# Kernel tuning notes

Hardware: AMD Instinct MI355X
Metric: run time of the kernel (lower is better)

## Reference

```python
import jax, jax.numpy as jnp
import numpy as np

B, L, D, N, KEEP, HID = 64, 256, 128, 8192, 64, 1024
IN_DIM = D + KEEP * D + 1  # q + packed subset keys + log_count


def setup_inputs() -> dict:
    key = jax.random.key(0)
    ks = jax.random.split(key, 7)
    q = jax.random.normal(ks[0], (N, D), jnp.float32)
    k = jax.random.normal(ks[1], (B, L, D), jnp.float32)
    batch_idx = jax.random.randint(ks[2], (N,), 0, B)
    mask = jax.random.randint(ks[3], (N, L), 0, 2).astype(bool)
    count = jax.random.randint(ks[4], (N,), 0, L)
    W1 = jax.random.normal(ks[5], (IN_DIM, HID), jnp.float32) / np.sqrt(IN_DIM).astype(np.float32)
    b1 = jnp.zeros((HID,), jnp.float32)
    W2 = jax.random.normal(ks[6], (HID, 1), jnp.float32) / np.sqrt(HID).astype(np.float32)
    b2 = jnp.zeros((1,), jnp.float32)
    return dict(q=q, k=k, batch_idx=batch_idx, mask=mask, count=count,
                W1=W1, b1=b1, W2=W2, b2=b2)


def _pack_subset_keys(k, batch_idx, mask):
    # chain_k: [N, L, D] gather of per-chain key blocks
    chain_k = k[batch_idx]
    pos = jnp.arange(L, dtype=jnp.float32)
    # score = L - pos for masked positions, 0 otherwise -> topk picks first KEEP masked positions
    scores = mask.astype(jnp.float32) * (jnp.float32(L) - pos)[None, :]
    top_scores, top_idx = jax.lax.top_k(scores, KEEP)
    picked = top_scores > 0
    sortable = jnp.where(picked, top_idx, L)  # sentinel L for unpicked
    sortable = jnp.sort(sortable, axis=1)     # restore ascending position order
    picked = sortable < L
    safe_idx = jnp.where(picked, sortable, 0)
    packed = jnp.take_along_axis(chain_k, safe_idx[:, :, None], axis=1)  # [N, KEEP, D]
    packed = packed * picked[:, :, None].astype(packed.dtype)
    return packed.reshape(N, KEEP * D)


def reference(q, k, batch_idx, mask, count, W1, b1, W2, b2):
    packed = _pack_subset_keys(k, batch_idx, mask)
    log_count = jnp.log1p(count.astype(q.dtype))[:, None]
    feat = jnp.concatenate([q, packed, log_count], axis=-1)  # [N, IN_DIM]
    h = jax.nn.gelu(feat @ W1 + b1, approximate=False)       # torch GELU = exact erf
    return (h @ W2 + b2).squeeze(-1)                          # [N]
```

## Files before the change

kernel.cpp:

```cpp
#include <hip/hip_runtime.h>
#include <math.h>

#define N_ROWS 8192
#define B_CH   64
#define L_SEQ  256
#define D_DIM  128
#define KEEP   64
#define HID    1024
#define KTOT   8320

#define KOFF   (N_ROWS * D_DIM)
#define ZOFF   (KOFF + B_CH * L_SEQ * D_DIM)
#define BUF_ELEMS (ZOFF + 128)

typedef unsigned short ushort_t;
typedef __attribute__((ext_vector_type(8))) short  short8;
typedef __attribute__((ext_vector_type(4))) float  float4v;


__device__ __forceinline__ ushort_t f2bf(float f) {
    union { float f; unsigned int u; } v; v.f = f;
    unsigned int u = v.u;
    unsigned int r = u + 0x7fffu + ((u >> 16) & 1u);
    return (ushort_t)(r >> 16);
}

__device__ __forceinline__ void glds16(const void* g, void* l) {
    __builtin_amdgcn_global_load_lds(
        (const __attribute__((address_space(1))) unsigned int*)g,
        (__attribute__((address_space(3))) unsigned int*)l,
        16, 0, 0);
}

__global__ void init_out(float* __restrict__ out, const float* __restrict__ b2) {
    int i = blockIdx.x * blockDim.x + threadIdx.x;
    if (i < N_ROWS) out[i] = b2[0];
}

__global__ void conv_qk(const float* __restrict__ q, const float* __restrict__ k,
                        ushort_t* __restrict__ buf) {
    int c = blockIdx.x * blockDim.x + threadIdx.x;
    if (c >= BUF_ELEMS / 8) return;
    int e = c * 8;
    float4 x0, x1;
    if (e < KOFF) {
        const float4* s = (const float4*)(q + e);
        x0 = s[0]; x1 = s[1];
    } else if (e < ZOFF) {
        const float4* s = (const float4*)(k + (e - KOFF));
        x0 = s[0]; x1 = s[1];
    } else {
        x0 = make_float4(0.f, 0.f, 0.f, 0.f);
        x1 = x0;
    }
    union { ushort_t s[8]; uint4 v; } o;
    o.s[0] = f2bf(x0.x); o.s[1] = f2bf(x0.y); o.s[2] = f2bf(x0.z); o.s[3] = f2bf(x0.w);
    o.s[4] = f2bf(x1.x); o.s[5] = f2bf(x1.y); o.s[6] = f2bf(x1.z); o.s[7] = f2bf(x1.w);
    *(uint4*)(buf + e) = o.v;
}

__global__ void conv_w1t(const float* __restrict__ W1, ushort_t* __restrict__ w1t) {
    __shared__ float tile[64][65];
    const int k0 = blockIdx.x * 64, h0 = blockIdx.y * 64;
    const int t = threadIdx.x;
    const int hl = t & 63, kl = t >> 6;
#pragma unroll
    for (int i = 0; i < 16; ++i) {
        int kk = kl + i * 4;
        tile[kk][hl] = W1[(size_t)(k0 + kk) * HID + h0 + hl];
    }
    __syncthreads();
#pragma unroll
    for (int i = 0; i < 2; ++i) {
        int chunk = i * 256 + t;
        int h = chunk >> 3, piece = chunk & 7;
        union { ushort_t s[8]; uint4 v; } o;
#pragma unroll
        for (int j = 0; j < 8; ++j) o.s[j] = f2bf(tile[piece * 8 + j][h]);
        *(uint4*)(w1t + (size_t)(h0 + h) * KTOT + k0 + piece * 8) = o.v;
    }
}

__global__ void pack_idx(const int* __restrict__ mask, const int* __restrict__ batch_idx,
                         const int* __restrict__ count, int* __restrict__ srcLUT,
                         float* __restrict__ logc) {
    const int n = blockIdx.x, t = threadIdx.x;
    __shared__ int sidx[KEEP];
    __shared__ int wcnt[4];
    if (t < KEEP) sidx[t] = -1;
    __syncthreads();
    const int m = (mask[n * L_SEQ + t] != 0) ? 1 : 0;
    unsigned long long bal = __ballot(m);
    const int w = t >> 6, l = t & 63;
    if (l == 0) wcnt[w] = (int)__popcll(bal);
    __syncthreads();
    int base = 0;
    for (int i = 0; i < w; ++i) base += wcnt[i];
    const int rank = base + (int)__popcll(bal & ((1ull << l) - 1ull));
    if (m && rank < KEEP) sidx[rank] = t;
    __syncthreads();
    if (t < KEEP) {
        int s = sidx[t];
        int b = batch_idx[n];
        srcLUT[(t + 1) * N_ROWS + n] = (s >= 0) ? (KOFF + (b * L_SEQ + s) * D_DIM) : ZOFF;
    }
    if (t == 64) logc[n] = log1pf((float)count[n]);
    if (t == 65) srcLUT[n] = n * D_DIM;
}

__global__ __launch_bounds__(256, 2)
void gemm_mlp(const ushort_t* __restrict__ buf, const ushort_t* __restrict__ w1t,
              const int* __restrict__ srcLUT, const float* __restrict__ logc,
              const float* __restrict__ W1, const float* __restrict__ b1,
              const float* __restrict__ W2, float* __restrict__ out) {
    __shared__ ushort_t As[128 * 128];
    __shared__ ushort_t Bs[128 * 128];

    const int t = threadIdx.x;
    const int blkM = blockIdx.x, blkH = blockIdx.y;
    const int wave = t >> 6, lane = t & 63;
    const int wm = wave >> 1, wh = wave & 1;
    const int ln = lane & 15, quad = lane >> 4;

    float4v acc[4][4];
#pragma unroll
    for (int i = 0; i < 4; ++i)
#pragma unroll
        for (int j = 0; j < 4; ++j)
#pragma unroll
            for (int r = 0; r < 4; ++r) acc[i][j][r] = 0.0f;

    const int tr = t >> 4;
    const int slot = t & 15;
    const int pg = slot ^ tr;
    ushort_t* lA = As + t * 8;
    ushort_t* lB = Bs + t * 8;
    const ushort_t* gB[8];
#pragma unroll
    for (int i = 0; i < 8; ++i)
        gB[i] = w1t + (size_t)(blkH * 128 + i * 16 + tr) * KTOT + pg * 8;
    const int* lutBase = srcLUT + blkM * 128 + tr;

    int offA[8];
#pragma unroll
    for (int i = 0; i < 8; ++i) offA[i] = lutBase[i * 16];

    for (int bi = 0; bi < 65; ++bi) {
#pragma unroll
        for (int i = 0; i < 8; ++i) {
            glds16(buf + offA[i] + pg * 8, lA + i * 2048);
            glds16(gB[i] + bi * 128, lB + i * 2048);
        }
        int offN[8];
        if (bi < 64) {
#pragma unroll
            for (int i = 0; i < 8; ++i) offN[i] = lutBase[(bi + 1) * N_ROWS + i * 16];
        }
        __syncthreads();
#pragma unroll
        for (int kk = 0; kk < 4; ++kk) {
            short8 af[4], bfr[4];
#pragma unroll
            for (int mi = 0; mi < 4; ++mi) {
                const int row = wm * 64 + mi * 16 + ln;
                const int sl = (kk * 4 + quad) ^ ln;
                af[mi] = *(const short8*)(As + row * 128 + sl * 8);
            }
#pragma unroll
            for (int ni = 0; ni < 4; ++ni) {
                const int row = wh * 64 + ni * 16 + ln;
                const int sl = (kk * 4 + quad) ^ ln;
                bfr[ni] = *(const short8*)(Bs + row * 128 + sl * 8);
            }
#pragma unroll
            for (int mi = 0; mi < 4; ++mi)
#pragma unroll
                for (int ni = 0; ni < 4; ++ni)
                    acc[mi][ni] = __builtin_amdgcn_mfma_f32_16x16x32_bf16(
                        af[mi], bfr[ni], acc[mi][ni], 0, 0, 0);
        }
        __syncthreads();
#pragma unroll
        for (int i = 0; i < 8; ++i) offA[i] = offN[i];
    }

    const float* w1last = W1 + (size_t)KTOT * HID;
    float w1l[4], b1v[4], w2v[4];
#pragma unroll
    for (int ni = 0; ni < 4; ++ni) {
        int h = blkH * 128 + wh * 64 + ni * 16 + ln;
        w1l[ni] = w1last[h];
        b1v[ni] = b1[h];
        w2v[ni] = W2[h];
    }
    const int nbase = blkM * 128 + wm * 64 + quad * 4;
#pragma unroll
    for (int mi = 0; mi < 4; ++mi) {
#pragma unroll
        for (int rg = 0; rg < 4; ++rg) {
            const int n = nbase + mi * 16 + rg;
            const float lc = logc[n];
            float s = 0.0f;
#pragma unroll
            for (int ni = 0; ni < 4; ++ni) {
                float pre = acc[mi][ni][rg] + lc * w1l[ni] + b1v[ni];
                float hv = 0.5f * pre * (1.0f + erff(pre * 0.70710678118654752f));
                s += hv * w2v[ni];
            }
            s += __shfl_xor(s, 1);
            s += __shfl_xor(s, 2);
            s += __shfl_xor(s, 4);
            s += __shfl_xor(s, 8);
            if (ln == 0) atomicAdd(out + n, s);
        }
    }
}

extern "C" void kernel_launch(void* const* d_in, const int* in_sizes, int n_in,
                              void* d_out, int out_size, void* d_ws, size_t ws_size,
                              hipStream_t stream) {
    const float* q     = (const float*)d_in[0];
    const float* k     = (const float*)d_in[1];
    const int*   bidx  = (const int*)d_in[2];
    const int*   mask  = (const int*)d_in[3];
    const int*   count = (const int*)d_in[4];
    const float* W1    = (const float*)d_in[5];
    const float* b1    = (const float*)d_in[6];
    const float* W2    = (const float*)d_in[7];
    const float* b2    = (const float*)d_in[8];
    float* out = (float*)d_out;

    char* ws = (char*)d_ws;
    ushort_t* buf    = (ushort_t*)(ws);
    ushort_t* w1t    = (ushort_t*)(ws + 6291712);
    int*      srcLUT = (int*)(ws + 6291712 + 17039360);
    float*    logc   = (float*)(ws + 6291712 + 17039360 + 2129920);

    init_out<<<(N_ROWS + 255) / 256, 256, 0, stream>>>(out, b2);
    conv_qk<<<(BUF_ELEMS / 8 + 255) / 256, 256, 0, stream>>>(q, k, buf);
    conv_w1t<<<dim3(KTOT / 64, HID / 64), 256, 0, stream>>>(W1, w1t);
    pack_idx<<<N_ROWS, 256, 0, stream>>>(mask, bidx, count, srcLUT, logc);
    gemm_mlp<<<dim3(N_ROWS / 128, HID / 128), 256, 0, stream>>>(
        buf, w1t, srcLUT, logc, W1, b1, W2, out);
}
```

Baseline: 259.4 us.

## Fuse preprocessing kernels into one launch and swap GEMM grid order

Merges init_out, conv_qk, conv_w1t and pack_idx into a single prep kernel that dispatches on block index, removing three launches and their serialization gaps. pack_idx is rewritten so each block handles 128 rows using ballot-based compaction, with a transposed LUT write that gives coalesced srcLUT stores. The GEMM grid is swapped so consecutive blocks share the same A rows across H tiles, aiming for better L2 reuse of gathered keys. The merged kernel uses a larger static shared allocation, which may reduce occupancy for the simple conversion blocks.

```diff
diff --git a/kernel.cpp b/kernel.cpp
--- a/kernel.cpp
+++ b/kernel.cpp
@@ -13,6 +13,12 @@
 #define ZOFF   (KOFF + B_CH * L_SEQ * D_DIM)
 #define BUF_ELEMS (ZOFF + 128)
 
+#define QK_BLOCKS   1537
+#define W1T_BLOCKS  2080
+#define PACK_BLOCKS 64
+#define OUT_BLOCKS  32
+#define PREP_GRID   (QK_BLOCKS + W1T_BLOCKS + PACK_BLOCKS + OUT_BLOCKS)
+
 typedef unsigned short ushort_t;
 typedef __attribute__((ext_vector_type(8))) short  short8;
 typedef __attribute__((ext_vector_type(4))) float  float4v;
@@ -32,80 +38,104 @@
         16, 0, 0);
 }
 
-__global__ void init_out(float* __restrict__ out, const float* __restrict__ b2) {
-    int i = blockIdx.x * blockDim.x + threadIdx.x;
-    if (i < N_ROWS) out[i] = b2[0];
-}
-
-__global__ void conv_qk(const float* __restrict__ q, const float* __restrict__ k,
-                        ushort_t* __restrict__ buf) {
-    int c = blockIdx.x * blockDim.x + threadIdx.x;
-    if (c >= BUF_ELEMS / 8) return;
-    int e = c * 8;
-    float4 x0, x1;
-    if (e < KOFF) {
-        const float4* s = (const float4*)(q + e);
-        x0 = s[0]; x1 = s[1];
-    } else if (e < ZOFF) {
-        const float4* s = (const float4*)(k + (e - KOFF));
-        x0 = s[0]; x1 = s[1];
+__global__ void prep(const float* __restrict__ q, const float* __restrict__ k,
+                     const float* __restrict__ W1, const int* __restrict__ mask,
+                     const int* __restrict__ batch_idx, const int* __restrict__ count,
+                     const float* __restrict__ b2,
+                     ushort_t* __restrict__ buf, ushort_t* __restrict__ w1t,
+                     int* __restrict__ srcLUT, float* __restrict__ logc,
+                     float* __restrict__ out) {
+    __shared__ __align__(16) char smem[34304];
+    const int blk = blockIdx.x;
+    const int t = threadIdx.x;
+
+    if (blk < QK_BLOCKS) {
+        int c = blk * 256 + t;
+        if (c >= BUF_ELEMS / 8) return;
+        int e = c * 8;
+        float4 x0, x1;
+        if (e < KOFF) {
+            const float4* s = (const float4*)(q + e);
+            x0 = s[0]; x1 = s[1];
+        } else if (e < ZOFF) {
+            const float4* s = (const float4*)(k + (e - KOFF));
+            x0 = s[0]; x1 = s[1];
+        } else {
+            x0 = make_float4(0.f, 0.f, 0.f, 0.f);
+            x1 = x0;
+        }
+        union { ushort_t s[8]; uint4 v; } o;
+        o.s[0] = f2bf(x0.x); o.s[1] = f2bf(x0.y); o.s[2] = f2bf(x0.z); o.s[3] = f2bf(x0.w);
+        o.s[4] = f2bf(x1.x); o.s[5] = f2bf(x1.y); o.s[6] = f2bf(x1.z); o.s[7] = f2bf(x1.w);
+        *(uint4*)(buf + e) = o.v;
+
+    } else if (blk < QK_BLOCKS + W1T_BLOCKS) {
+        const int idx = blk - QK_BLOCKS;
+        const int k0 = (idx % 130) * 64, h0 = (idx / 130) * 64;
+        float (*tile)[65] = (float(*)[65])smem;
+        const int hl = t & 63, kl = t >> 6;
+#pragma unroll
+        for (int i = 0; i < 16; ++i) {
+            int kk = kl + i * 4;
+            tile[kk][hl] = W1[(size_t)(k0 + kk) * HID + h0 + hl];
+        }
+        __syncthreads();
+#pragma unroll
+        for (int i = 0; i < 2; ++i) {
+            int chunk = i * 256 + t;
+            int h = chunk >> 3, piece = chunk & 7;
+            union { ushort_t s[8]; uint4 v; } o;
+#pragma unroll
+            for (int j = 0; j < 8; ++j) o.s[j] = f2bf(tile[piece * 8 + j][h]);
+            *(uint4*)(w1t + (size_t)(h0 + h) * KTOT + k0 + piece * 8) = o.v;
+        }
+
+    } else if (blk < QK_BLOCKS + W1T_BLOCKS + PACK_BLOCKS) {
+        const int p = blk - (QK_BLOCKS + W1T_BLOCKS);
+        const int n0 = p * 128;
+        int* sidx = (int*)smem;
+        int* bidx_l = (int*)(smem + 33280);
+        for (int i = t; i < 128 * 65; i += 256) sidx[i] = -1;
+        if (t < 128) {
+            int n = n0 + t;
+            bidx_l[t] = batch_idx[n];
+            logc[n] = log1pf((float)count[n]);
+            srcLUT[n] = n * D_DIM;
+        }
+        __syncthreads();
+        const int w = t >> 6, l = t & 63;
+        const unsigned long long ltm = (1ull << l) - 1ull;
+        for (int r = 0; r < 32; ++r) {
+            const int lr = w * 32 + r;
+            const int n = n0 + lr;
+            const int* mrow = mask + (size_t)n * L_SEQ;
+            int m0 = mrow[l] != 0;
+            int m1 = mrow[64 + l] != 0;
+            int m2 = mrow[128 + l] != 0;
+            int m3 = mrow[192 + l] != 0;
+            unsigned long long b0 = __ballot(m0), b1 = __ballot(m1);
+            unsigned long long b2v = __ballot(m2), b3 = __ballot(m3);
+            int p1 = (int)__popcll(b0);
+            int p2 = p1 + (int)__popcll(b1);
+            int p3 = p2 + (int)__popcll(b2v);
+            int* row = sidx + lr * 65;
+            if (m0) { int rk = (int)__popcll(b0 & ltm);      if (rk < KEEP) row[rk] = l; }
+            if (m1) { int rk = p1 + (int)__popcll(b1 & ltm); if (rk < KEEP) row[rk] = 64 + l; }
+            if (m2) { int rk = p2 + (int)__popcll(b2v & ltm); if (rk < KEEP) row[rk] = 128 + l; }
+            if (m3) { int rk = p3 + (int)__popcll(b3 & ltm); if (rk < KEEP) row[rk] = 192 + l; }
+        }
+        __syncthreads();
+        for (int e = t; e < KEEP * 128; e += 256) {
+            int j = e >> 7, nl = e & 127;
+            int s = sidx[nl * 65 + j];
+            srcLUT[(size_t)(j + 1) * N_ROWS + n0 + nl] =
+                (s >= 0) ? (KOFF + (bidx_l[nl] * L_SEQ + s) * D_DIM) : ZOFF;
+        }
+
     } else {
-        x0 = make_float4(0.f, 0.f, 0.f, 0.f);
-        x1 = x0;
-    }
-    union { ushort_t s[8]; uint4 v; } o;
-    o.s[0] = f2bf(x0.x); o.s[1] = f2bf(x0.y); o.s[2] = f2bf(x0.z); o.s[3] = f2bf(x0.w);
-    o.s[4] = f2bf(x1.x); o.s[5] = f2bf(x1.y); o.s[6] = f2bf(x1.z); o.s[7] = f2bf(x1.w);
-    *(uint4*)(buf + e) = o.v;
-}
-
-__global__ void conv_w1t(const float* __restrict__ W1, ushort_t* __restrict__ w1t) {
-    __shared__ float tile[64][65];
-    const int k0 = blockIdx.x * 64, h0 = blockIdx.y * 64;
-    const int t = threadIdx.x;
-    const int hl = t & 63, kl = t >> 6;
-#pragma unroll
-    for (int i = 0; i < 16; ++i) {
-        int kk = kl + i * 4;
-        tile[kk][hl] = W1[(size_t)(k0 + kk) * HID + h0 + hl];
-    }
-    __syncthreads();
-#pragma unroll
-    for (int i = 0; i < 2; ++i) {
-        int chunk = i * 256 + t;
-        int h = chunk >> 3, piece = chunk & 7;
-        union { ushort_t s[8]; uint4 v; } o;
-#pragma unroll
-        for (int j = 0; j < 8; ++j) o.s[j] = f2bf(tile[piece * 8 + j][h]);
-        *(uint4*)(w1t + (size_t)(h0 + h) * KTOT + k0 + piece * 8) = o.v;
-    }
-}
-
-__global__ void pack_idx(const int* __restrict__ mask, const int* __restrict__ batch_idx,
-                         const int* __restrict__ count, int* __restrict__ srcLUT,
-                         float* __restrict__ logc) {
-    const int n = blockIdx.x, t = threadIdx.x;
-    __shared__ int sidx[KEEP];
-    __shared__ int wcnt[4];
-    if (t < KEEP) sidx[t] = -1;
-    __syncthreads();
-    const int m = (mask[n * L_SEQ + t] != 0) ? 1 : 0;
-    unsigned long long bal = __ballot(m);
-    const int w = t >> 6, l = t & 63;
-    if (l == 0) wcnt[w] = (int)__popcll(bal);
-    __syncthreads();
-    int base = 0;
-    for (int i = 0; i < w; ++i) base += wcnt[i];
-    const int rank = base + (int)__popcll(bal & ((1ull << l) - 1ull));
-    if (m && rank < KEEP) sidx[rank] = t;
-    __syncthreads();
-    if (t < KEEP) {
-        int s = sidx[t];
-        int b = batch_idx[n];
-        srcLUT[(t + 1) * N_ROWS + n] = (s >= 0) ? (KOFF + (b * L_SEQ + s) * D_DIM) : ZOFF;
-    }
-    if (t == 64) logc[n] = log1pf((float)count[n]);
-    if (t == 65) srcLUT[n] = n * D_DIM;
+        int i = (blk - (QK_BLOCKS + W1T_BLOCKS + PACK_BLOCKS)) * 256 + t;
+        if (i < N_ROWS) out[i] = b2[0];
+    }
 }
 
 __global__ __launch_bounds__(256, 2)
@@ -117,7 +147,7 @@
     __shared__ ushort_t Bs[128 * 128];
 
     const int t = threadIdx.x;
-    const int blkM = blockIdx.x, blkH = blockIdx.y;
+    const int blkH = blockIdx.x, blkM = blockIdx.y;
     const int wave = t >> 6, lane = t & 63;
     const int wm = wave >> 1, wh = wave & 1;
     const int ln = lane & 15, quad = lane >> 4;
@@ -236,10 +266,8 @@
     int*      srcLUT = (int*)(ws + 6291712 + 17039360);
     float*    logc   = (float*)(ws + 6291712 + 17039360 + 2129920);
 
-    init_out<<<(N_ROWS + 255) / 256, 256, 0, stream>>>(out, b2);
-    conv_qk<<<(BUF_ELEMS / 8 + 255) / 256, 256, 0, stream>>>(q, k, buf);
-    conv_w1t<<<dim3(KTOT / 64, HID / 64), 256, 0, stream>>>(W1, w1t);
-    pack_idx<<<N_ROWS, 256, 0, stream>>>(mask, bidx, count, srcLUT, logc);
-    gemm_mlp<<<dim3(N_ROWS / 128, HID / 128), 256, 0, stream>>>(
+    prep<<<PREP_GRID, 256, 0, stream>>>(q, k, W1, mask, bidx, count, b2,
+                                        buf, w1t, srcLUT, logc, out);
+    gemm_mlp<<<dim3(HID / 128, N_ROWS / 128), 256, 0, stream>>>(
         buf, w1t, srcLUT, logc, W1, b1, W2, out);
 }
```

Measured after the change: 268.7 us. +3.6%, slower.
